# Kernel tuning notes

Hardware: AMD Instinct MI355X
Metric: run time of the kernel (lower is better)

## Reference

```python
import jax, jax.numpy as jnp
import numpy as np

EPS = 1e-5

def _act_quant(x):
    # per-token absmax int8 quantization (BitNet b1.58)
    scale = 127.0 / jnp.clip(jnp.max(jnp.abs(x), axis=-1, keepdims=True), EPS)
    return jnp.clip(jnp.round(x * scale), -128.0, 127.0) / scale

def _weight_quant(w):
    # per-tensor absmean ternary quantization {-1, 0, +1}
    scale = 1.0 / jnp.clip(jnp.mean(jnp.abs(w)), EPS)
    return jnp.clip(jnp.round(w * scale), -1.0, 1.0) / scale

def _bitlinear(x, w):
    # STE: forward uses quantized values, gradient passes through
    xq = x + jax.lax.stop_gradient(_act_quant(x) - x)
    wq = w + jax.lax.stop_gradient(_weight_quant(w) - w)
    # torch Linear: y = x @ W.T, W is [out, in]
    return jnp.einsum('bsd,od->bso', xq, wq)

def setup_inputs() -> dict:
    key = jax.random.key(0)
    k1, k2, k3, k4 = jax.random.split(key, 4)
    B, S, D = 8, 2048, 512
    x = jax.random.normal(k1, (B, S, D), dtype=jnp.float32)
    s = (1.0 / D) ** 0.5
    Wq = jax.random.normal(k2, (D, D), dtype=jnp.float32) * s
    Wk = jax.random.normal(k3, (D, D), dtype=jnp.float32) * s
    Wv = jax.random.normal(k4, (D, D), dtype=jnp.float32) * s
    return {"x": x, "Wq": Wq, "Wk": Wk, "Wv": Wv}

def reference(x, Wq, Wk, Wv):
    B, S, D = x.shape
    q = _bitlinear(x, Wq)
    k = _bitlinear(x, Wk)
    v = _bitlinear(x, Wv)
    # NOTE: original scales by batch_size**-0.5 (faithful to source)
    scores = jnp.einsum('bqd,bkd->bqk', q, k) * (B ** -0.5)
    causal = jnp.tril(jnp.ones((S, S), dtype=bool))  # tril[:S, :S]
    scores = jnp.where(causal, scores, -jnp.inf)
    attn = jax.nn.softmax(scores, axis=-1)
    return jnp.einsum('bqk,bkd->bqd', attn, v)
```

## Files before the change

### kernel.cpp

```cpp
#include <hip/hip_runtime.h>
#include <cstdint>
#include <cstddef>

#define BATCH 8
#define SEQ   2048
#define DDIM  512
#define NROW  (BATCH*SEQ)
#define KPACK (DDIM/4)
#define EPSQ  1e-5f
#define FSCALE 0.35355339059327373f

typedef _Float16 half8 __attribute__((ext_vector_type(8)));
typedef _Float16 half4 __attribute__((ext_vector_type(4)));
typedef float    f32x4 __attribute__((ext_vector_type(4)));
typedef int      i32x4 __attribute__((ext_vector_type(4)));

static constexpr size_t OFF_M   = 0;
static constexpr size_t OFF_WP  = 256;
static constexpr size_t OFF_XQ  = OFF_WP + (size_t)3*KPACK*DDIM*4;
static constexpr size_t OFF_SX  = OFF_XQ + (size_t)NROW*KPACK*4;
static constexpr size_t OFF_QKV = OFF_SX + (size_t)NROW*4;
static constexpr size_t OFF_PO  = OFF_QKV + (size_t)3*NROW*DDIM*2;
static constexpr size_t OFF_PM  = OFF_PO + (size_t)512*64*512*4;
static constexpr size_t OFF_PL  = OFF_PM + (size_t)512*64*4;

__device__ __forceinline__ int q8(float v, float s) {
  int i = (int)rintf(v * s);
  i = i < -128 ? -128 : (i > 127 ? 127 : i);
  return i & 0xff;
}

__device__ __forceinline__ void gld_lds16(const _Float16* g, _Float16* l) {
  __builtin_amdgcn_global_load_lds(
      (const __attribute__((address_space(1))) void*)g,
      (__attribute__((address_space(3))) void*)l, 16, 0, 0);
}

__global__ __launch_bounds__(256) void wsum_kernel(
    const float* __restrict__ Wq, const float* __restrict__ Wk,
    const float* __restrict__ Wv, float* __restrict__ mw) {
  const float* W = blockIdx.y == 0 ? Wq : (blockIdx.y == 1 ? Wk : Wv);
  __shared__ float red[256];
  const float4* p = (const float4*)(W + blockIdx.x * 8192);
  float s = 0.f;
  #pragma unroll
  for (int i = 0; i < 8; i++) {
    float4 a = p[i * 256 + threadIdx.x];
    s += fabsf(a.x) + fabsf(a.y) + fabsf(a.z) + fabsf(a.w);
  }
  red[threadIdx.x] = s;
  __syncthreads();
  for (int w = 128; w > 0; w >>= 1) {
    if ((int)threadIdx.x < w) red[threadIdx.x] += red[threadIdx.x + w];
    __syncthreads();
  }
  if (threadIdx.x == 0) atomicAdd(&mw[blockIdx.y], red[0]);
}

__global__ __launch_bounds__(256) void wquant_kernel(
    const float* __restrict__ Wq, const float* __restrict__ Wk,
    const float* __restrict__ Wv, const float* __restrict__ mw,
    int* __restrict__ wp) {
  int idx = blockIdx.x * 256 + threadIdx.x;
  int mat = idx >> 16;
  int local = idx & 0xFFFF;
  int o  = local >> 7;
  int k4 = local & 127;
  const float* W = mat == 0 ? Wq : (mat == 1 ? Wk : Wv);
  float mean = mw[mat] * (1.0f / 262144.0f);
  float scale = 1.0f / fmaxf(mean, EPSQ);
  float4 w4 = *(const float4*)(W + (size_t)o * DDIM + k4 * 4);
  int t0 = (int)rintf(w4.x * scale); t0 = t0 < -1 ? -1 : (t0 > 1 ? 1 : t0);
  int t1 = (int)rintf(w4.y * scale); t1 = t1 < -1 ? -1 : (t1 > 1 ? 1 : t1);
  int t2 = (int)rintf(w4.z * scale); t2 = t2 < -1 ? -1 : (t2 > 1 ? 1 : t2);
  int t3 = (int)rintf(w4.w * scale); t3 = t3 < -1 ? -1 : (t3 > 1 ? 1 : t3);
  int packed = (t0 & 0xff) | ((t1 & 0xff) << 8) | ((t2 & 0xff) << 16) | ((t3 & 0xff) << 24);
  wp[((size_t)mat * DDIM + o) * KPACK + k4] = packed;
}

__global__ __launch_bounds__(256) void aquant_kernel(
    const float* __restrict__ x, int* __restrict__ xq, float* __restrict__ sx) {
  int wid = threadIdx.x >> 6, lane = threadIdx.x & 63;
  int row = blockIdx.x * 4 + wid;
  const float* xr = x + (size_t)row * DDIM;
  float4 a = ((const float4*)xr)[lane];
  float4 b = ((const float4*)xr)[64 + lane];
  float amax = fmaxf(fmaxf(fmaxf(fabsf(a.x), fabsf(a.y)), fmaxf(fabsf(a.z), fabsf(a.w))),
                     fmaxf(fmaxf(fabsf(b.x), fabsf(b.y)), fmaxf(fabsf(b.z), fabsf(b.w))));
  for (int off = 32; off > 0; off >>= 1) amax = fmaxf(amax, __shfl_xor(amax, off, 64));
  float aa = fmaxf(amax, EPSQ);
  float scale = 127.0f / aa;
  int p0 = q8(a.x, scale) | (q8(a.y, scale) << 8) | (q8(a.z, scale) << 16) | (q8(a.w, scale) << 24);
  int p1 = q8(b.x, scale) | (q8(b.y, scale) << 8) | (q8(b.z, scale) << 16) | (q8(b.w, scale) << 24);
  xq[(size_t)row * KPACK + lane]      = p0;
  xq[(size_t)row * KPACK + 64 + lane] = p1;
  if (lane == 0) sx[row] = aa * (1.0f / 127.0f);
}

__global__ __launch_bounds__(256, 2) void qkv_gemm_kernel(
    const int* __restrict__ xq, const int* __restrict__ wp,
    const float* __restrict__ sx, const float* __restrict__ mw,
    _Float16* __restrict__ qkv) {
  __shared__ __align__(16) int xs[64][132];
  __shared__ __align__(16) int bs[64][132];
  __shared__ float sxs[64];

  const int tid  = threadIdx.x;
  const int w    = tid >> 6;
  const int lane = tid & 63;
  const int quad = lane >> 4;
  const int col  = lane & 15;

  const int r0g = blockIdx.x * 64;
  const int n0  = blockIdx.y * 64;
  const int mat = blockIdx.z;

  {
    const i32x4* src = (const i32x4*)(xq + (size_t)r0g * KPACK);
    #pragma unroll
    for (int i = 0; i < 8; i++) {
      int e = i * 256 + tid;
      int row = e >> 5, u = e & 31;
      *(i32x4*)&xs[row][u * 4] = src[e];
    }
  }
  {
    const i32x4* src = (const i32x4*)(wp + ((size_t)mat * DDIM + n0) * KPACK);
    #pragma unroll
    for (int i = 0; i < 8; i++) {
      int e = i * 256 + tid;
      int c = e >> 5, u = e & 31;
      *(i32x4*)&bs[c][u * 4] = src[e];
    }
  }
  if (tid < 64) sxs[tid] = sx[r0g + tid];
  __syncthreads();

  i32x4 acc[4];
  #pragma unroll
  for (int rt = 0; rt < 4; rt++) acc[rt] = (i32x4)(0);

  #pragma unroll
  for (int s = 0; s < 8; s++) {
    i32x4 bf = *(const i32x4*)&bs[w * 16 + col][s * 16 + quad * 4];
    #pragma unroll
    for (int rt = 0; rt < 4; rt++) {
      i32x4 af = *(const i32x4*)&xs[rt * 16 + col][s * 16 + quad * 4];
      acc[rt] = __builtin_amdgcn_mfma_i32_16x16x64_i8(af, bf, acc[rt], 0, 0, 0);
    }
  }

  const float mval = fmaxf(mw[mat] * (1.0f / 262144.0f), EPSQ);
  const int nw = n0 + w * 16 + col;

  if (mat < 2) {
    _Float16* outb = qkv + (size_t)mat * NROW * DDIM;
    #pragma unroll
    for (int rt = 0; rt < 4; rt++) {
      #pragma unroll
      for (int reg = 0; reg < 4; reg++) {
        int rowl = rt * 16 + quad * 4 + reg;
        outb[(size_t)(r0g + rowl) * DDIM + nw] =
            (_Float16)((float)acc[rt][reg] * sxs[rowl] * mval);
      }
    }
  } else {
    _Float16* vT = qkv + (size_t)2 * NROW * DDIM;
    #pragma unroll
    for (int rt = 0; rt < 4; rt++) {
      half4 hv;
      #pragma unroll
      for (int reg = 0; reg < 4; reg++) {
        int rowl = rt * 16 + quad * 4 + reg;
        hv[reg] = (_Float16)((float)acc[rt][reg] * sxs[rowl] * mval);
      }
      int r = r0g + rt * 16 + quad * 4;
      int b = r >> 11, kt = (r & 2047) >> 5, kin = r & 31;
      *(half4*)(vT + ((((size_t)b * 64 + kt) * 512 + nw) * 32 + kin)) = hv;
    }
  }
}

__global__ __launch_bounds__(512, 2) void flash_kernel(
    const _Float16* __restrict__ q, const _Float16* __restrict__ k,
    const _Float16* __restrict__ vT, _Float16* __restrict__ po,
    float* __restrict__ pm, float* __restrict__ pl) {
  __shared__ __align__(16) _Float16 Ksh[2][32][520];
  __shared__ __align__(16) _Float16 VtL[2][512][32];
  __shared__ __align__(16) float    PsS[64 * 33];
  __shared__ __align__(16) _Float16 Pf[64 * 40];
  __shared__ float alpha_l[64];

  const int tid  = threadIdx.x;
  const int w    = tid >> 6;
  const int lane = tid & 63;
  const int quad = lane >> 4;
  const int col  = lane & 15;
  const int rt   = w & 3;
  const int kh   = w >> 2;
  const int smrow = tid >> 3;
  const int sme   = tid & 7;
  const int d0  = w * 64;

  const int vrl = lane >> 2;
  const int vu  = lane & 3;

  const int bb = blockIdx.x & 7;
  const int qi = blockIdx.x >> 3;

  for (int ph = 0; ph < 2; ph++) {
    const int qt = ph ? (31 - qi) : qi;
    const int h  = ph;
    const int slot = ((qt * 8 + bb) * 2 + h);
    const int nT = qt + 1;

    const int qrow0 = qt * 64;
    const size_t bbase = (size_t)bb * SEQ * DDIM;
    const _Float16* kb_p = k + bbase;
    const _Float16* vt_p = vT + (size_t)bb * 64 * 512 * 32;

    half8 qfrag[16];
    {
      const _Float16* qrow_p = q + bbase + (size_t)(qrow0 + rt * 16 + col) * DDIM;
      #pragma unroll
      for (int s = 0; s < 16; s++)
        qfrag[s] = *(const half8*)(qrow_p + s * 32 + quad * 8);
    }

    float m_run = -INFINITY, l_run = 0.f;
    f32x4 o[4][4];
    #pragma unroll
    for (int a = 0; a < 4; a++)
      #pragma unroll
      for (int b2 = 0; b2 < 4; b2++) o[a][b2] = (f32x4)(0.f);

    #pragma unroll
    for (int i = 0; i < 4; i++)
      gld_lds16(kb_p + (size_t)(h * 32 + w * 4 + i) * DDIM + lane * 8,
                &Ksh[0][w * 4 + i][0]);
    {
      const _Float16* vtile = vt_p + (size_t)h * 512 * 32;
      #pragma unroll
      for (int i = 0; i < 4; i++) {
        int r = w * 64 + i * 16 + vrl;
        int su = vu ^ ((r >> 1) & 3);
        gld_lds16(vtile + (size_t)r * 32 + su * 8, &VtL[0][w * 64 + i * 16][0]);
      }
    }
    __syncthreads();

    for (int t = 0; t < nT; t++) {
      const int cur = t & 1, nxt = cur ^ 1;
      const int kb0 = (2 * t + h) * 32;

      if (t + 1 < nT) {
        const int kb1 = kb0 + 64;
        #pragma unroll
        for (int i = 0; i < 4; i++)
          gld_lds16(kb_p + (size_t)(kb1 + w * 4 + i) * DDIM + lane * 8,
                    &Ksh[nxt][w * 4 + i][0]);
        const _Float16* vtile = vt_p + (size_t)(2 * t + h + 2) * 512 * 32;
        #pragma unroll
        for (int i = 0; i < 4; i++) {
          int r = w * 64 + i * 16 + vrl;
          int su = vu ^ ((r >> 1) & 3);
          gld_lds16(vtile + (size_t)r * 32 + su * 8, &VtL[nxt][w * 64 + i * 16][0]);
        }
      }

      {
        f32x4 c = (f32x4)(0.f);
        #pragma unroll
        for (int s = 0; s < 16; s++) {
          half8 b = *(const half8*)&Ksh[cur][kh * 16 + col][s * 32 + quad * 8];
          c = __builtin_amdgcn_mfma_f32_16x16x32_f16(qfrag[s], b, c, 0, 0, 0);
        }
        #pragma unroll
        for (int reg = 0; reg < 4; reg++)
          PsS[(rt * 16 + quad * 4 + reg) * 33 + kh * 16 + col] = c[reg];
      }
      __syncthreads();

      {
        const int qrow = qrow0 + smrow;
        float sv[4];
        #pragma unroll
        for (int i = 0; i < 4; i++) {
          float s = PsS[smrow * 33 + sme * 4 + i] * FSCALE;
          if (kb0 + sme * 4 + i > qrow) s = -INFINITY;
          sv[i] = s;
        }
        float mx = fmaxf(fmaxf(sv[0], sv[1]), fmaxf(sv[2], sv[3]));
        #pragma unroll
        for (int m = 1; m <= 4; m <<= 1) mx = fmaxf(mx, __shfl_xor(mx, m, 64));
        float mn = fmaxf(m_run, mx);
        float mnc = fmaxf(mn, -1e30f);
        float al = __expf(m_run - mnc);
        half4 p4;
        float rs = 0.f;
        #pragma unroll
        for (int i = 0; i < 4; i++) {
          float p = __expf(sv[i] - mnc);
          rs += p;
          p4[i] = (_Float16)p;
        }
        #pragma unroll
        for (int m = 1; m <= 4; m <<= 1) rs += __shfl_xor(rs, m, 64);
        l_run = l_run * al + rs;
        m_run = mn;
        *(half4*)&Pf[smrow * 40 + sme * 4] = p4;
        if (sme == 0) alpha_l[smrow] = al;
      }
      __syncthreads();

      {
        half8 ap[4];
        f32x4 af[4];
        #pragma unroll
        for (int r2 = 0; r2 < 4; r2++) {
          ap[r2] = *(const half8*)&Pf[(r2 * 16 + col) * 40 + quad * 8];
          af[r2] = *(const f32x4*)&alpha_l[r2 * 16 + quad * 4];
        }
        #pragma unroll
        for (int r2 = 0; r2 < 4; r2++)
          #pragma unroll
          for (int ct = 0; ct < 4; ct++)
            o[r2][ct] *= af[r2];
        #pragma unroll
        for (int ct = 0; ct < 4; ct++) {
          int R = d0 + ct * 16 + col;
          int ur = quad ^ ((R >> 1) & 3);
          half8 bv = *(const half8*)&VtL[cur][R][ur * 8];
          #pragma unroll
          for (int r2 = 0; r2 < 4; r2++)
            o[r2][ct] = __builtin_amdgcn_mfma_f32_16x16x32_f16(ap[r2], bv, o[r2][ct], 0, 0, 0);
        }
      }
      __syncthreads();
    }

    if (sme == 0) {
      pm[slot * 64 + smrow] = m_run;
      pl[slot * 64 + smrow] = l_run;
    }
    {
      _Float16* pob = po + (size_t)slot * 64 * 512;
      #pragma unroll
      for (int r2 = 0; r2 < 4; r2++) {
        #pragma unroll
        for (int ct = 0; ct < 4; ct++) {
          #pragma unroll
          for (int e = 0; e < 4; e++) {
            __builtin_nontemporal_store(
                (_Float16)o[r2][ct][e],
                &pob[(size_t)(r2 * 16 + quad * 4 + e) * 512 + d0 + ct * 16 + col]);
          }
        }
      }
    }
  }
}

__global__ __launch_bounds__(256) void merge_kernel(
    const _Float16* __restrict__ po, const float* __restrict__ pm,
    const float* __restrict__ pl, float* __restrict__ out) {
  __shared__ float w0s[64], w1s[64], dns[64];
  const int tid = threadIdx.x;
  const int qt = blockIdx.x, b = blockIdx.y;
  const int slot0 = (qt * 8 + b) * 2;
  const int slot1 = slot0 + 1;

  if (tid < 64) {
    float m0 = pm[slot0 * 64 + tid], m1 = pm[slot1 * 64 + tid];
    float l0 = pl[slot0 * 64 + tid], l1 = pl[slot1 * 64 + tid];
    float ms = fmaxf(m0, m1);
    float a0 = __expf(m0 - ms);
    float a1 = __expf(m1 - ms);
    w0s[tid] = a0;
    w1s[tid] = a1;
    dns[tid] = 1.0f / (a0 * l0 + a1 * l1);
  }
  __syncthreads();

  const half8* p0 = (const half8*)(po + (size_t)slot0 * 64 * 512);
  const half8* p1 = (const half8*)(po + (size_t)slot1 * 64 * 512);
  f32x4* op = (f32x4*)(out + ((size_t)b * SEQ + qt * 64) * 512);
  #pragma unroll 4
  for (int j = 0; j < 16; j++) {
    int e = j * 256 + tid;
    int row = e >> 6;
    half8 a = __builtin_nontemporal_load(p0 + e);
    half8 c = __builtin_nontemporal_load(p1 + e);
    float w0 = w0s[row], w1 = w1s[row], dn = dns[row];
    f32x4 r0, r1;
    #pragma unroll
    for (int u = 0; u < 4; u++) r0[u] = ((float)a[u] * w0 + (float)c[u] * w1) * dn;
    #pragma unroll
    for (int u = 0; u < 4; u++) r1[u] = ((float)a[4 + u] * w0 + (float)c[4 + u] * w1) * dn;
    op[e * 2]     = r0;
    op[e * 2 + 1] = r1;
  }
}

extern "C" void kernel_launch(void* const* d_in, const int* in_sizes, int n_in,
                              void* d_out, int out_size, void* d_ws, size_t ws_size,
                              hipStream_t stream) {
  const float* x  = (const float*)d_in[0];
  const float* Wq = (const float*)d_in[1];
  const float* Wk = (const float*)d_in[2];
  const float* Wv = (const float*)d_in[3];
  float* out = (float*)d_out;
  char* ws = (char*)d_ws;

  float* mw  = (float*)(ws + OFF_M);
  int*   wp  = (int*)(ws + OFF_WP);
  int*   xq  = (int*)(ws + OFF_XQ);
  float* sx  = (float*)(ws + OFF_SX);
  _Float16* qkv = (_Float16*)(ws + OFF_QKV);
  _Float16* qf  = qkv;
  _Float16* kf  = qkv + (size_t)NROW * DDIM;
  _Float16* vTf = qkv + 2 * (size_t)NROW * DDIM;
  _Float16* po = (_Float16*)(ws + OFF_PO);
  float* pm = (float*)(ws + OFF_PM);
  float* pl = (float*)(ws + OFF_PL);

  hipMemsetAsync(mw, 0, 16, stream);
  wsum_kernel<<<dim3(32, 3), 256, 0, stream>>>(Wq, Wk, Wv, mw);
  wquant_kernel<<<768, 256, 0, stream>>>(Wq, Wk, Wv, mw, wp);
  aquant_kernel<<<4096, 256, 0, stream>>>(x, xq, sx);
  qkv_gemm_kernel<<<dim3(256, 8, 3), 256, 0, stream>>>(xq, wp, sx, mw, qkv);
  flash_kernel<<<dim3(256), 512, 0, stream>>>(qf, kf, vTf, po, pm, pl);
  merge_kernel<<<dim3(32, 8), 256, 0, stream>>>(po, pm, pl, out);
}
```

Measured before the change: 226.5 us.

## Fuse prep kernels, loop GEMM over N tiles, replace flash barriers with waitcnt

The weight-sum and activation-quant kernels are merged into one launch. The QKV GEMM block now loops over all eight N tiles, reusing the X tile held in LDS and prefetching the next weight tile into registers. The flash kernel swaps __syncthreads for explicit vmcnt/lgkmcnt waits plus barriers, so the async K/V prefetch can stay in flight, and it raises wave priority around the MFMA sections. The cost is fewer GEMM blocks (768 vs 6144), which lowers parallelism, plus hand-tuned waitcnt counts that must match the number of outstanding loads.

```diff
diff --git a/kernel.cpp b/kernel.cpp
--- a/kernel.cpp
+++ b/kernel.cpp
@@ -24,6 +24,11 @@
 static constexpr size_t OFF_PM  = OFF_PO + (size_t)512*64*512*4;
 static constexpr size_t OFF_PL  = OFF_PM + (size_t)512*64*4;
 
+#define VM8()   asm volatile("s_waitcnt vmcnt(8)" ::: "memory")
+#define VM0()   asm volatile("s_waitcnt vmcnt(0)" ::: "memory")
+#define LGKM0() asm volatile("s_waitcnt lgkmcnt(0)" ::: "memory")
+#define BAR()   __builtin_amdgcn_s_barrier()
+
 __device__ __forceinline__ int q8(float v, float s) {
   int i = (int)rintf(v * s);
   i = i < -128 ? -128 : (i > 127 ? 127 : i);
@@ -36,25 +41,47 @@
       (__attribute__((address_space(3))) void*)l, 16, 0, 0);
 }
 
-__global__ __launch_bounds__(256) void wsum_kernel(
+__global__ __launch_bounds__(256) void prep_kernel(
     const float* __restrict__ Wq, const float* __restrict__ Wk,
-    const float* __restrict__ Wv, float* __restrict__ mw) {
-  const float* W = blockIdx.y == 0 ? Wq : (blockIdx.y == 1 ? Wk : Wv);
-  __shared__ float red[256];
-  const float4* p = (const float4*)(W + blockIdx.x * 8192);
-  float s = 0.f;
-  #pragma unroll
-  for (int i = 0; i < 8; i++) {
-    float4 a = p[i * 256 + threadIdx.x];
-    s += fabsf(a.x) + fabsf(a.y) + fabsf(a.z) + fabsf(a.w);
-  }
-  red[threadIdx.x] = s;
-  __syncthreads();
-  for (int w = 128; w > 0; w >>= 1) {
-    if ((int)threadIdx.x < w) red[threadIdx.x] += red[threadIdx.x + w];
+    const float* __restrict__ Wv, float* __restrict__ mw,
+    const float* __restrict__ x, int* __restrict__ xq,
+    float* __restrict__ sx) {
+  if (blockIdx.x < 96) {
+    const int mat = blockIdx.x >> 5;
+    const int bx  = blockIdx.x & 31;
+    const float* W = mat == 0 ? Wq : (mat == 1 ? Wk : Wv);
+    __shared__ float red[256];
+    const float4* p = (const float4*)(W + bx * 8192);
+    float s = 0.f;
+    #pragma unroll
+    for (int i = 0; i < 8; i++) {
+      float4 a = p[i * 256 + threadIdx.x];
+      s += fabsf(a.x) + fabsf(a.y) + fabsf(a.z) + fabsf(a.w);
+    }
+    red[threadIdx.x] = s;
     __syncthreads();
-  }
-  if (threadIdx.x == 0) atomicAdd(&mw[blockIdx.y], red[0]);
+    for (int w = 128; w > 0; w >>= 1) {
+      if ((int)threadIdx.x < w) red[threadIdx.x] += red[threadIdx.x + w];
+      __syncthreads();
+    }
+    if (threadIdx.x == 0) atomicAdd(&mw[mat], red[0]);
+  } else {
+    int wid = threadIdx.x >> 6, lane = threadIdx.x & 63;
+    int row = (blockIdx.x - 96) * 4 + wid;
+    const float* xr = x + (size_t)row * DDIM;
+    float4 a = ((const float4*)xr)[lane];
+    float4 b = ((const float4*)xr)[64 + lane];
+    float amax = fmaxf(fmaxf(fmaxf(fabsf(a.x), fabsf(a.y)), fmaxf(fabsf(a.z), fabsf(a.w))),
+                       fmaxf(fmaxf(fabsf(b.x), fabsf(b.y)), fmaxf(fabsf(b.z), fabsf(b.w))));
+    for (int off = 32; off > 0; off >>= 1) amax = fmaxf(amax, __shfl_xor(amax, off, 64));
+    float aa = fmaxf(amax, EPSQ);
+    float scale = 127.0f / aa;
+    int p0 = q8(a.x, scale) | (q8(a.y, scale) << 8) | (q8(a.z, scale) << 16) | (q8(a.w, scale) << 24);
+    int p1 = q8(b.x, scale) | (q8(b.y, scale) << 8) | (q8(b.z, scale) << 16) | (q8(b.w, scale) << 24);
+    xq[(size_t)row * KPACK + lane]      = p0;
+    xq[(size_t)row * KPACK + 64 + lane] = p1;
+    if (lane == 0) sx[row] = aa * (1.0f / 127.0f);
+  }
 }
 
 __global__ __launch_bounds__(256) void wquant_kernel(
@@ -78,25 +105,6 @@
   wp[((size_t)mat * DDIM + o) * KPACK + k4] = packed;
 }
 
-__global__ __launch_bounds__(256) void aquant_kernel(
-    const float* __restrict__ x, int* __restrict__ xq, float* __restrict__ sx) {
-  int wid = threadIdx.x >> 6, lane = threadIdx.x & 63;
-  int row = blockIdx.x * 4 + wid;
-  const float* xr = x + (size_t)row * DDIM;
-  float4 a = ((const float4*)xr)[lane];
-  float4 b = ((const float4*)xr)[64 + lane];
-  float amax = fmaxf(fmaxf(fmaxf(fabsf(a.x), fabsf(a.y)), fmaxf(fabsf(a.z), fabsf(a.w))),
-                     fmaxf(fmaxf(fabsf(b.x), fabsf(b.y)), fmaxf(fabsf(b.z), fabsf(b.w))));
-  for (int off = 32; off > 0; off >>= 1) amax = fmaxf(amax, __shfl_xor(amax, off, 64));
-  float aa = fmaxf(amax, EPSQ);
-  float scale = 127.0f / aa;
-  int p0 = q8(a.x, scale) | (q8(a.y, scale) << 8) | (q8(a.z, scale) << 16) | (q8(a.w, scale) << 24);
-  int p1 = q8(b.x, scale) | (q8(b.y, scale) << 8) | (q8(b.z, scale) << 16) | (q8(b.w, scale) << 24);
-  xq[(size_t)row * KPACK + lane]      = p0;
-  xq[(size_t)row * KPACK + 64 + lane] = p1;
-  if (lane == 0) sx[row] = aa * (1.0f / 127.0f);
-}
-
 __global__ __launch_bounds__(256, 2) void qkv_gemm_kernel(
     const int* __restrict__ xq, const int* __restrict__ wp,
     const float* __restrict__ sx, const float* __restrict__ mw,
@@ -112,8 +120,7 @@
   const int col  = lane & 15;
 
   const int r0g = blockIdx.x * 64;
-  const int n0  = blockIdx.y * 64;
-  const int mat = blockIdx.z;
+  const int mat = blockIdx.y;
 
   {
     const i32x4* src = (const i32x4*)(xq + (size_t)r0g * KPACK);
@@ -124,59 +131,74 @@
       *(i32x4*)&xs[row][u * 4] = src[e];
     }
   }
+  if (tid < 64) sxs[tid] = sx[r0g + tid];
+
+  const float mval = fmaxf(mw[mat] * (1.0f / 262144.0f), EPSQ);
+
+  i32x4 breg[8];
   {
-    const i32x4* src = (const i32x4*)(wp + ((size_t)mat * DDIM + n0) * KPACK);
+    const i32x4* src = (const i32x4*)(wp + (size_t)mat * DDIM * KPACK);
+    #pragma unroll
+    for (int i = 0; i < 8; i++) breg[i] = src[i * 256 + tid];
+  }
+
+  for (int nb = 0; nb < 8; nb++) {
+    const int n0 = nb * 64;
+    __syncthreads();
     #pragma unroll
     for (int i = 0; i < 8; i++) {
       int e = i * 256 + tid;
       int c = e >> 5, u = e & 31;
-      *(i32x4*)&bs[c][u * 4] = src[e];
-    }
-  }
-  if (tid < 64) sxs[tid] = sx[r0g + tid];
-  __syncthreads();
-
-  i32x4 acc[4];
-  #pragma unroll
-  for (int rt = 0; rt < 4; rt++) acc[rt] = (i32x4)(0);
-
-  #pragma unroll
-  for (int s = 0; s < 8; s++) {
-    i32x4 bf = *(const i32x4*)&bs[w * 16 + col][s * 16 + quad * 4];
-    #pragma unroll
-    for (int rt = 0; rt < 4; rt++) {
-      i32x4 af = *(const i32x4*)&xs[rt * 16 + col][s * 16 + quad * 4];
-      acc[rt] = __builtin_amdgcn_mfma_i32_16x16x64_i8(af, bf, acc[rt], 0, 0, 0);
-    }
-  }
-
-  const float mval = fmaxf(mw[mat] * (1.0f / 262144.0f), EPSQ);
-  const int nw = n0 + w * 16 + col;
-
-  if (mat < 2) {
-    _Float16* outb = qkv + (size_t)mat * NROW * DDIM;
-    #pragma unroll
-    for (int rt = 0; rt < 4; rt++) {
-      #pragma unroll
-      for (int reg = 0; reg < 4; reg++) {
-        int rowl = rt * 16 + quad * 4 + reg;
-        outb[(size_t)(r0g + rowl) * DDIM + nw] =
-            (_Float16)((float)acc[rt][reg] * sxs[rowl] * mval);
-      }
-    }
-  } else {
-    _Float16* vT = qkv + (size_t)2 * NROW * DDIM;
-    #pragma unroll
-    for (int rt = 0; rt < 4; rt++) {
-      half4 hv;
-      #pragma unroll
-      for (int reg = 0; reg < 4; reg++) {
-        int rowl = rt * 16 + quad * 4 + reg;
-        hv[reg] = (_Float16)((float)acc[rt][reg] * sxs[rowl] * mval);
-      }
-      int r = r0g + rt * 16 + quad * 4;
-      int b = r >> 11, kt = (r & 2047) >> 5, kin = r & 31;
-      *(half4*)(vT + ((((size_t)b * 64 + kt) * 512 + nw) * 32 + kin)) = hv;
+      *(i32x4*)&bs[c][u * 4] = breg[i];
+    }
+    __syncthreads();
+    if (nb + 1 < 8) {
+      const i32x4* src = (const i32x4*)(wp + ((size_t)mat * DDIM + n0 + 64) * KPACK);
+      #pragma unroll
+      for (int i = 0; i < 8; i++) breg[i] = src[i * 256 + tid];
+    }
+
+    i32x4 acc[4];
+    #pragma unroll
+    for (int rt = 0; rt < 4; rt++) acc[rt] = (i32x4)(0);
+
+    #pragma unroll
+    for (int s = 0; s < 8; s++) {
+      i32x4 bf = *(const i32x4*)&bs[w * 16 + col][s * 16 + quad * 4];
+      #pragma unroll
+      for (int rt = 0; rt < 4; rt++) {
+        i32x4 af = *(const i32x4*)&xs[rt * 16 + col][s * 16 + quad * 4];
+        acc[rt] = __builtin_amdgcn_mfma_i32_16x16x64_i8(af, bf, acc[rt], 0, 0, 0);
+      }
+    }
+
+    const int nw = n0 + w * 16 + col;
+
+    if (mat < 2) {
+      _Float16* outb = qkv + (size_t)mat * NROW * DDIM;
+      #pragma unroll
+      for (int rt = 0; rt < 4; rt++) {
+        #pragma unroll
+        for (int reg = 0; reg < 4; reg++) {
+          int rowl = rt * 16 + quad * 4 + reg;
+          outb[(size_t)(r0g + rowl) * DDIM + nw] =
+              (_Float16)((float)acc[rt][reg] * sxs[rowl] * mval);
+        }
+      }
+    } else {
+      _Float16* vT = qkv + (size_t)2 * NROW * DDIM;
+      #pragma unroll
+      for (int rt = 0; rt < 4; rt++) {
+        half4 hv;
+        #pragma unroll
+        for (int reg = 0; reg < 4; reg++) {
+          int rowl = rt * 16 + quad * 4 + reg;
+          hv[reg] = (_Float16)((float)acc[rt][reg] * sxs[rowl] * mval);
+        }
+        int r = r0g + rt * 16 + quad * 4;
+        int b = r >> 11, kt = (r & 2047) >> 5, kin = r & 31;
+        *(half4*)(vT + ((((size_t)b * 64 + kt) * 512 + nw) * 32 + kin)) = hv;
+      }
     }
   }
 }
@@ -211,7 +233,7 @@
   for (int ph = 0; ph < 2; ph++) {
     const int qt = ph ? (31 - qi) : qi;
     const int h  = ph;
-    const int slot = ((qt * 8 + bb) * 2 + h);
+    const int slot = (qt * 8 + bb) * 2 + h;
     const int nT = qt + 1;
 
     const int qrow0 = qt * 64;
@@ -247,7 +269,6 @@
         gld_lds16(vtile + (size_t)r * 32 + su * 8, &VtL[0][w * 64 + i * 16][0]);
       }
     }
-    __syncthreads();
 
     for (int t = 0; t < nT; t++) {
       const int cur = t & 1, nxt = cur ^ 1;
@@ -267,19 +288,24 @@
           gld_lds16(vtile + (size_t)r * 32 + su * 8, &VtL[nxt][w * 64 + i * 16][0]);
         }
       }
+      if (t + 1 < nT) { VM8(); } else { VM0(); }
+      BAR();
+      __builtin_amdgcn_sched_barrier(0);
 
       {
         f32x4 c = (f32x4)(0.f);
+        __builtin_amdgcn_s_setprio(1);
         #pragma unroll
         for (int s = 0; s < 16; s++) {
           half8 b = *(const half8*)&Ksh[cur][kh * 16 + col][s * 32 + quad * 8];
           c = __builtin_amdgcn_mfma_f32_16x16x32_f16(qfrag[s], b, c, 0, 0, 0);
         }
+        __builtin_amdgcn_s_setprio(0);
         #pragma unroll
         for (int reg = 0; reg < 4; reg++)
           PsS[(rt * 16 + quad * 4 + reg) * 33 + kh * 16 + col] = c[reg];
       }
-      __syncthreads();
+      LGKM0(); BAR();
 
       {
         const int qrow = qrow0 + smrow;
@@ -311,7 +337,7 @@
         *(half4*)&Pf[smrow * 40 + sme * 4] = p4;
         if (sme == 0) alpha_l[smrow] = al;
       }
-      __syncthreads();
+      LGKM0(); BAR();
 
       {
         half8 ap[4];
@@ -326,6 +352,7 @@
           #pragma unroll
           for (int ct = 0; ct < 4; ct++)
             o[r2][ct] *= af[r2];
+        __builtin_amdgcn_s_setprio(1);
         #pragma unroll
         for (int ct = 0; ct < 4; ct++) {
           int R = d0 + ct * 16 + col;
@@ -335,8 +362,9 @@
           for (int r2 = 0; r2 < 4; r2++)
             o[r2][ct] = __builtin_amdgcn_mfma_f32_16x16x32_f16(ap[r2], bv, o[r2][ct], 0, 0, 0);
         }
-      }
-      __syncthreads();
+        __builtin_amdgcn_s_setprio(0);
+      }
+      LGKM0(); BAR();
     }
 
     if (sme == 0) {
@@ -425,10 +453,9 @@
   float* pl = (float*)(ws + OFF_PL);
 
   hipMemsetAsync(mw, 0, 16, stream);
-  wsum_kernel<<<dim3(32, 3), 256, 0, stream>>>(Wq, Wk, Wv, mw);
+  prep_kernel<<<4192, 256, 0, stream>>>(Wq, Wk, Wv, mw, x, xq, sx);
   wquant_kernel<<<768, 256, 0, stream>>>(Wq, Wk, Wv, mw, wp);
-  aquant_kernel<<<4096, 256, 0, stream>>>(x, xq, sx);
-  qkv_gemm_kernel<<<dim3(256, 8, 3), 256, 0, stream>>>(xq, wp, sx, mw, qkv);
+  qkv_gemm_kernel<<<dim3(256, 3), 256, 0, stream>>>(xq, wp, sx, mw, qkv);
   flash_kernel<<<dim3(256), 512, 0, stream>>>(qf, kf, vTf, po, pm, pl);
   merge_kernel<<<dim3(32, 8), 256, 0, stream>>>(po, pm, pl, out);
 }
```

Result: faster. 217.9 us (-3.8%).
